# Kernel tuning notes

Measured on AMD Instinct MI355X. Metric: run time of the kernel, lower is better.

Reference implementation:

```python
import jax, jax.numpy as jnp
import numpy as np

FEATURE_DIM, HIDDEN_DIM, ATTN_DIM = 2048, 1024, 1024
B, L = 128, 196


def setup_inputs() -> dict:
    key = jax.random.key(0)
    ks = jax.random.split(key, 8)
    s_enc = 1.0 / np.sqrt(FEATURE_DIM)
    s_hid = 1.0 / np.sqrt(HIDDEN_DIM)
    s_full = 1.0 / np.sqrt(ATTN_DIM)
    return {
        "encoder_out": jax.random.normal(ks[0], (B, L, FEATURE_DIM), jnp.float32),
        "hidden": jax.random.normal(ks[1], (B, HIDDEN_DIM), jnp.float32),
        "W_enc": jax.random.uniform(ks[2], (FEATURE_DIM, ATTN_DIM), jnp.float32, -s_enc, s_enc),
        "b_enc": jax.random.uniform(ks[3], (ATTN_DIM,), jnp.float32, -s_enc, s_enc),
        "W_hid": jax.random.uniform(ks[4], (HIDDEN_DIM, ATTN_DIM), jnp.float32, -s_hid, s_hid),
        "b_hid": jax.random.uniform(ks[5], (ATTN_DIM,), jnp.float32, -s_hid, s_hid),
        "W_full": jax.random.uniform(ks[6], (ATTN_DIM,), jnp.float32, -s_full, s_full),
        "b_full": jax.random.uniform(ks[7], (1,), jnp.float32, -s_full, s_full),
    }


def reference(encoder_out, hidden, W_enc, b_enc, W_hid, b_hid, W_full, b_full):
    # attn1: (B, L, A)
    attn1 = jnp.einsum("blf,fa->bla", encoder_out, W_enc) + b_enc
    # attn2: (B, 1, A)
    attn2 = (hidden @ W_hid + b_hid)[:, None, :]
    attn = jax.nn.relu(attn1 + attn2)
    # scalar score per location: (B, L)
    scores = jnp.einsum("bla,a->bl", attn, W_full) + b_full[0]
    alpha = jax.nn.softmax(scores, axis=1)
    # weighted sum over L: (B, F)
    context = jnp.einsum("blf,bl->bf", encoder_out, alpha)
    return context, alpha
```

## Files before the change

kernel.cpp:

```cpp
#include <hip/hip_runtime.h>
#include <hip/hip_bf16.h>

typedef unsigned short u16;
typedef short s16x8 __attribute__((ext_vector_type(8)));
typedef unsigned int u32x4 __attribute__((ext_vector_type(4)));
typedef float f32x4 __attribute__((ext_vector_type(4)));

#define F_DIM 2048
#define A_DIM 1024
#define H_DIM 1024
#define BATCH 128
#define LLEN  196
#define MROWS (BATCH * LLEN)

__device__ __forceinline__ u16 f2b(float x) {
  union { float f; unsigned int u; } c; c.f = x;
  unsigned int r = (c.u + 0x7fffu + ((c.u >> 16) & 1u)) >> 16;
  return (u16)r;
}

__device__ __forceinline__ unsigned int f2b_pk(float a, float b) {
  unsigned int r;
  asm volatile("v_cvt_pk_bf16_f32 %0, %1, %2" : "=v"(r) : "v"(a), "v"(b));
  return r;
}

__device__ __forceinline__ void gload_lds16(const void* g, void* l) {
  __builtin_amdgcn_global_load_lds((const __attribute__((address_space(1))) void*)g,
                                   (__attribute__((address_space(3))) void*)l, 16, 0, 0);
}

__global__ void wenc_cvt_kernel(const float* __restrict__ W, u16* __restrict__ WT) {
  __shared__ float tile[32][33];
  int kb = blockIdx.x * 32, ab = blockIdx.y * 32;
  int t = threadIdx.x;
  int r = t >> 3, c = (t & 7) * 4;
  float4 v = *(const float4*)&W[(size_t)(kb + r) * A_DIM + ab + c];
  tile[r][c] = v.x; tile[r][c + 1] = v.y; tile[r][c + 2] = v.z; tile[r][c + 3] = v.w;
  __syncthreads();
  ushort4 o;
  o.x = f2b(tile[c + 0][r]);
  o.y = f2b(tile[c + 1][r]);
  o.z = f2b(tile[c + 2][r]);
  o.w = f2b(tile[c + 3][r]);
  *(ushort4*)&WT[(size_t)(ab + r) * F_DIM + kb + c] = o;
}

__global__ void attn2_kernel(const float* __restrict__ hidden, const float* __restrict__ W_hid,
                             const float* __restrict__ b_hid, const float* __restrict__ b_enc,
                             float* __restrict__ attn2p) {
  __shared__ float hl[8][128];
  int t = threadIdx.x;
  int a  = blockIdx.x * 256 + t;
  int b0 = blockIdx.y * 8;
  int k0 = blockIdx.z * 128;
  {
    int j = t >> 5, kk = (t & 31) * 4;
    float4 v = *(const float4*)&hidden[(size_t)(b0 + j) * H_DIM + k0 + kk];
    hl[j][kk + 0] = v.x; hl[j][kk + 1] = v.y; hl[j][kk + 2] = v.z; hl[j][kk + 3] = v.w;
  }
  __syncthreads();
  float acc[8] = {0.f, 0.f, 0.f, 0.f, 0.f, 0.f, 0.f, 0.f};
  #pragma unroll 4
  for (int k = 0; k < 128; ++k) {
    float w = W_hid[(size_t)(k0 + k) * A_DIM + a];
    #pragma unroll
    for (int j = 0; j < 8; ++j) acc[j] = fmaf(hl[j][k], w, acc[j]);
  }
  if (blockIdx.z == 0) {
    float bias = b_hid[a] + b_enc[a];
    #pragma unroll
    for (int j = 0; j < 8; ++j) acc[j] += bias;
  }
  #pragma unroll
  for (int j = 0; j < 8; ++j) atomicAdd(&attn2p[(size_t)(b0 + j) * A_DIM + a], acc[j]);
}

__global__ void gemm_score(const float* __restrict__ enc, const u16* __restrict__ WT,
                           const float* __restrict__ attn2p, const float* __restrict__ W_full,
                           float* __restrict__ scores) {
  __shared__ __align__(16) float Asf[128 * 32];
  __shared__ __align__(16) u16 Bs[128 * 32];
  __shared__ float wf_lds[128];
  __shared__ float at2_lds[2][128];

  int i = blockIdx.x;
  int g  = i >> 6;
  int r  = i & 63;
  int y  = r >> 3;
  int gi = r & 7;
  int mt = g * 8 + gi;
  if (mt >= MROWS / 128) return;

  int n0 = y * 128;
  int m0 = mt * 128;
  int t = threadIdx.x;

  int b0 = m0 / LLEN;
  int bnd = (b0 + 1) * LLEN;
  int b1 = min(b0 + 1, BATCH - 1);

  if (t < 128) {
    wf_lds[t] = W_full[n0 + t];
    at2_lds[0][t] = attn2p[(size_t)b0 * A_DIM + n0 + t];
    at2_lds[1][t] = attn2p[(size_t)b1 * A_DIM + n0 + t];
  }

  int lane = t & 63, wave = t >> 6;
  int wr = wave >> 1, wc = wave & 1;
  int c16 = lane & 15, quad = lane >> 4;

  f32x4 acc[4][4];
  #pragma unroll
  for (int ii = 0; ii < 4; ++ii)
    #pragma unroll
    for (int j = 0; j < 4; ++j) acc[ii][j] = (f32x4){0.f, 0.f, 0.f, 0.f};

  const float* agp = enc + (size_t)(m0 + wave * 32 + (lane >> 3)) * F_DIM
                         + ((lane & 7) ^ ((lane >> 3) & 7)) * 4;
  float* al = Asf + wave * 1024;
  const u16* bgp = WT + (size_t)(n0 + (t >> 2)) * F_DIM + ((t & 3) ^ ((t >> 3) & 3)) * 8;
  u16* bl = Bs + wave * 512;

  int akey = c16 & 7;
  int bkey = (c16 >> 1) & 3;

  for (int kt = 0; kt < F_DIM; kt += 32) {
    gload_lds16(agp + kt, al);
    gload_lds16(agp + (size_t)8 * F_DIM + kt, al + 256);
    gload_lds16(agp + (size_t)16 * F_DIM + kt, al + 512);
    gload_lds16(agp + (size_t)24 * F_DIM + kt, al + 768);
    gload_lds16(bgp + kt, bl);
    gload_lds16(bgp + (size_t)64 * F_DIM + kt, bl + 2048);
    __syncthreads();
    s16x8 af[4], bf[4];
    #pragma unroll
    for (int ii = 0; ii < 4; ++ii) {
      int arow = (wr * 64 + ii * 16 + c16) * 32;
      float4 lo = *(const float4*)&Asf[arow + ((2 * quad) ^ akey) * 4];
      float4 hi = *(const float4*)&Asf[arow + ((2 * quad + 1) ^ akey) * 4];
      u32x4 w;
      w.x = f2b_pk(lo.x, lo.y);
      w.y = f2b_pk(lo.z, lo.w);
      w.z = f2b_pk(hi.x, hi.y);
      w.w = f2b_pk(hi.z, hi.w);
      af[ii] = __builtin_bit_cast(s16x8, w);
      bf[ii] = *(const s16x8*)&Bs[(wc * 64 + ii * 16 + c16) * 32 + (quad ^ bkey) * 8];
    }
    #pragma unroll
    for (int mi = 0; mi < 4; ++mi)
      #pragma unroll
      for (int ni = 0; ni < 4; ++ni)
        acc[mi][ni] = __builtin_amdgcn_mfma_f32_16x16x32_bf16(af[mi], bf[ni], acc[mi][ni], 0, 0, 0);
    __syncthreads();
  }

  float wf[4], a2a[4], a2b[4];
  #pragma unroll
  for (int ni = 0; ni < 4; ++ni) {
    int col = wc * 64 + ni * 16 + c16;
    wf[ni] = wf_lds[col];
    a2a[ni] = at2_lds[0][col];
    a2b[ni] = at2_lds[1][col];
  }
  #pragma unroll
  for (int mi = 0; mi < 4; ++mi) {
    #pragma unroll
    for (int rr = 0; rr < 4; ++rr) {
      int row_g = m0 + wr * 64 + mi * 16 + quad * 4 + rr;
      bool hi = row_g >= bnd;
      float p = 0.f;
      #pragma unroll
      for (int ni = 0; ni < 4; ++ni) {
        float v = acc[mi][ni][rr] + (hi ? a2b[ni] : a2a[ni]);
        v = fmaxf(v, 0.f);
        p = fmaf(v, wf[ni], p);
      }
      p += __shfl_xor(p, 1);
      p += __shfl_xor(p, 2);
      p += __shfl_xor(p, 4);
      p += __shfl_xor(p, 8);
      if (c16 == 0) atomicAdd(&scores[row_g], p);
    }
  }
}

__global__ void softmax_kernel(const float* __restrict__ scores, float* __restrict__ alpha) {
  __shared__ float red[8];
  int b = blockIdx.x, t = threadIdx.x;
  float s = (t < LLEN) ? scores[b * LLEN + t] : -3.0e38f;
  float m = s;
  #pragma unroll
  for (int o = 1; o <= 32; o <<= 1) m = fmaxf(m, __shfl_xor(m, o));
  if ((t & 63) == 0) red[t >> 6] = m;
  __syncthreads();
  m = fmaxf(fmaxf(red[0], red[1]), fmaxf(red[2], red[3]));
  float e = (t < LLEN) ? expf(s - m) : 0.f;
  float sum = e;
  #pragma unroll
  for (int o = 1; o <= 32; o <<= 1) sum += __shfl_xor(sum, o);
  __syncthreads();
  if ((t & 63) == 0) red[4 + (t >> 6)] = sum;
  __syncthreads();
  sum = red[4] + red[5] + red[6] + red[7];
  if (t < LLEN) alpha[b * LLEN + t] = e / sum;
}

__global__ void context_kernel(const float* __restrict__ enc, const float* __restrict__ alpha,
                               float* __restrict__ out) {
  __shared__ float al[49];
  int b = blockIdx.y, t = threadIdx.x;
  int l0 = blockIdx.z * 49;
  int f4 = blockIdx.x * 256 + t;
  if (t < 49) al[t] = alpha[b * LLEN + l0 + t];
  __syncthreads();
  const float4* e4 = (const float4*)enc + ((size_t)b * LLEN + l0) * (F_DIM / 4) + f4;
  float4 acc = {0.f, 0.f, 0.f, 0.f};
  #pragma unroll 7
  for (int l = 0; l < 49; ++l) {
    float4 v = e4[(size_t)l * (F_DIM / 4)];
    float a = al[l];
    acc.x = fmaf(v.x, a, acc.x);
    acc.y = fmaf(v.y, a, acc.y);
    acc.z = fmaf(v.z, a, acc.z);
    acc.w = fmaf(v.w, a, acc.w);
  }
  float* o = out + (size_t)b * F_DIM + f4 * 4;
  atomicAdd(o + 0, acc.x);
  atomicAdd(o + 1, acc.y);
  atomicAdd(o + 2, acc.z);
  atomicAdd(o + 3, acc.w);
}

extern "C" void kernel_launch(void* const* d_in, const int* in_sizes, int n_in,
                              void* d_out, int out_size, void* d_ws, size_t ws_size,
                              hipStream_t stream) {
  const float* enc    = (const float*)d_in[0];
  const float* hidden = (const float*)d_in[1];
  const float* W_enc  = (const float*)d_in[2];
  const float* b_enc  = (const float*)d_in[3];
  const float* W_hid  = (const float*)d_in[4];
  const float* b_hid  = (const float*)d_in[5];
  const float* W_full = (const float*)d_in[6];
  float* out = (float*)d_out;
  float* alpha_out = out + (size_t)BATCH * F_DIM;

  const size_t wt_bytes = (size_t)A_DIM * F_DIM * sizeof(u16);
  const size_t a2_bytes = (size_t)BATCH * A_DIM * sizeof(float);
  const size_t sc_bytes = (size_t)MROWS * sizeof(float);
  char* ws = (char*)d_ws;
  u16*   WT     = (u16*)ws;
  float* attn2p = (float*)(ws + wt_bytes);
  float* scores = (float*)(ws + wt_bytes + a2_bytes);

  hipMemsetAsync(attn2p, 0, a2_bytes, stream);
  hipMemsetAsync(scores, 0, sc_bytes, stream);
  hipMemsetAsync(out, 0, (size_t)BATCH * F_DIM * sizeof(float), stream);

  wenc_cvt_kernel<<<dim3(F_DIM / 32, A_DIM / 32), 256, 0, stream>>>(W_enc, WT);
  attn2_kernel<<<dim3(A_DIM / 256, BATCH / 8, H_DIM / 128), 256, 0, stream>>>(hidden, W_hid, b_hid, b_enc, attn2p);
  gemm_score<<<dim3(1600), 256, 0, stream>>>(enc, WT, attn2p, W_full, scores);
  softmax_kernel<<<dim3(BATCH), 256, 0, stream>>>(scores, alpha_out);
  context_kernel<<<dim3(2, BATCH, 4), 256, 0, stream>>>(enc, alpha_out, out);
}
```

Measured before the change: 500.2 us.

## Merge prep kernels and memsets, convert A tile in registers, fuse softmax into context

The W_enc transpose, the attn2 GEMV (now full-K per block with no atomics), and zeroing of scores and out are merged into one prep kernel in place of separate launches and memsets. gemm_score now loads encoder rows into registers, converts them to bf16 and stores them to LDS, instead of using an async fp32 global-to-LDS copy with conversion at fragment load. The LDS XOR swizzles are removed. Softmax is fused into the context kernel, which recomputes it per block, cutting launch count and the alpha round trip. The risks are exposed global-load latency in the GEMM without async LDS loads, possible LDS bank conflicts without swizzling, and a less parallel attn2 (64 blocks doing full K).

```diff
diff --git a/kernel.cpp b/kernel.cpp
--- a/kernel.cpp
+++ b/kernel.cpp
@@ -13,6 +13,12 @@
 #define LLEN  196
 #define MROWS (BATCH * LLEN)
 
+#define PREP_WENC   2048
+#define PREP_ATTN2  (PREP_WENC + 64)
+#define PREP_ZSC    (PREP_ATTN2 + 25)
+#define PREP_ZOUT   (PREP_ZSC + 256)
+#define PREP_GRID   PREP_ZOUT
+
 __device__ __forceinline__ u16 f2b(float x) {
   union { float f; unsigned int u; } c; c.f = x;
   unsigned int r = (c.u + 0x7fffu + ((c.u >> 16) & 1u)) >> 16;
@@ -30,56 +36,60 @@
                                    (__attribute__((address_space(3))) void*)l, 16, 0, 0);
 }
 
-__global__ void wenc_cvt_kernel(const float* __restrict__ W, u16* __restrict__ WT) {
+__global__ void prep_kernel(const float* __restrict__ W, u16* __restrict__ WT,
+                            const float* __restrict__ hidden, const float* __restrict__ W_hid,
+                            const float* __restrict__ b_hid, const float* __restrict__ b_enc,
+                            float* __restrict__ attn2p, float* __restrict__ scores,
+                            float* __restrict__ out) {
   __shared__ float tile[32][33];
-  int kb = blockIdx.x * 32, ab = blockIdx.y * 32;
-  int t = threadIdx.x;
-  int r = t >> 3, c = (t & 7) * 4;
-  float4 v = *(const float4*)&W[(size_t)(kb + r) * A_DIM + ab + c];
-  tile[r][c] = v.x; tile[r][c + 1] = v.y; tile[r][c + 2] = v.z; tile[r][c + 3] = v.w;
-  __syncthreads();
-  ushort4 o;
-  o.x = f2b(tile[c + 0][r]);
-  o.y = f2b(tile[c + 1][r]);
-  o.z = f2b(tile[c + 2][r]);
-  o.w = f2b(tile[c + 3][r]);
-  *(ushort4*)&WT[(size_t)(ab + r) * F_DIM + kb + c] = o;
-}
-
-__global__ void attn2_kernel(const float* __restrict__ hidden, const float* __restrict__ W_hid,
-                             const float* __restrict__ b_hid, const float* __restrict__ b_enc,
-                             float* __restrict__ attn2p) {
-  __shared__ float hl[8][128];
-  int t = threadIdx.x;
-  int a  = blockIdx.x * 256 + t;
-  int b0 = blockIdx.y * 8;
-  int k0 = blockIdx.z * 128;
-  {
-    int j = t >> 5, kk = (t & 31) * 4;
-    float4 v = *(const float4*)&hidden[(size_t)(b0 + j) * H_DIM + k0 + kk];
-    hl[j][kk + 0] = v.x; hl[j][kk + 1] = v.y; hl[j][kk + 2] = v.z; hl[j][kk + 3] = v.w;
-  }
-  __syncthreads();
-  float acc[8] = {0.f, 0.f, 0.f, 0.f, 0.f, 0.f, 0.f, 0.f};
-  #pragma unroll 4
-  for (int k = 0; k < 128; ++k) {
-    float w = W_hid[(size_t)(k0 + k) * A_DIM + a];
-    #pragma unroll
-    for (int j = 0; j < 8; ++j) acc[j] = fmaf(hl[j][k], w, acc[j]);
-  }
-  if (blockIdx.z == 0) {
+  __shared__ float hl[8][1024];
+  int bid = blockIdx.x, t = threadIdx.x;
+
+  if (bid < PREP_WENC) {
+    int kb = (bid & 63) * 32, ab = (bid >> 6) * 32;
+    int r = t >> 3, c = (t & 7) * 4;
+    float4 v = *(const float4*)&W[(size_t)(kb + r) * A_DIM + ab + c];
+    tile[r][c] = v.x; tile[r][c + 1] = v.y; tile[r][c + 2] = v.z; tile[r][c + 3] = v.w;
+    __syncthreads();
+    ushort4 o;
+    o.x = f2b(tile[c + 0][r]);
+    o.y = f2b(tile[c + 1][r]);
+    o.z = f2b(tile[c + 2][r]);
+    o.w = f2b(tile[c + 3][r]);
+    *(ushort4*)&WT[(size_t)(ab + r) * F_DIM + kb + c] = o;
+  } else if (bid < PREP_ATTN2) {
+    int idx = bid - PREP_WENC;
+    int a  = (idx & 3) * 256 + t;
+    int b0 = (idx >> 2) * 8;
+    #pragma unroll
+    for (int j = 0; j < 8; ++j) {
+      float4 v = *(const float4*)&hidden[(size_t)(b0 + j) * H_DIM + t * 4];
+      *(float4*)&hl[j][t * 4] = v;
+    }
+    __syncthreads();
+    float acc[8] = {0.f, 0.f, 0.f, 0.f, 0.f, 0.f, 0.f, 0.f};
+    #pragma unroll 8
+    for (int k = 0; k < H_DIM; ++k) {
+      float w = W_hid[(size_t)k * A_DIM + a];
+      #pragma unroll
+      for (int j = 0; j < 8; ++j) acc[j] = fmaf(hl[j][k], w, acc[j]);
+    }
     float bias = b_hid[a] + b_enc[a];
     #pragma unroll
-    for (int j = 0; j < 8; ++j) acc[j] += bias;
-  }
-  #pragma unroll
-  for (int j = 0; j < 8; ++j) atomicAdd(&attn2p[(size_t)(b0 + j) * A_DIM + a], acc[j]);
+    for (int j = 0; j < 8; ++j) attn2p[(size_t)(b0 + j) * A_DIM + a] = acc[j] + bias;
+  } else if (bid < PREP_ZSC) {
+    int i4 = (bid - PREP_ATTN2) * 256 + t;
+    if (i4 < MROWS / 4) ((float4*)scores)[i4] = (float4){0.f, 0.f, 0.f, 0.f};
+  } else {
+    int i4 = (bid - PREP_ZSC) * 256 + t;
+    ((float4*)out)[i4] = (float4){0.f, 0.f, 0.f, 0.f};
+  }
 }
 
 __global__ void gemm_score(const float* __restrict__ enc, const u16* __restrict__ WT,
                            const float* __restrict__ attn2p, const float* __restrict__ W_full,
                            float* __restrict__ scores) {
-  __shared__ __align__(16) float Asf[128 * 32];
+  __shared__ __align__(16) u16 As[128 * 32];
   __shared__ __align__(16) u16 Bs[128 * 32];
   __shared__ float wf_lds[128];
   __shared__ float at2_lds[2][128];
@@ -116,36 +126,31 @@
     #pragma unroll
     for (int j = 0; j < 4; ++j) acc[ii][j] = (f32x4){0.f, 0.f, 0.f, 0.f};
 
-  const float* agp = enc + (size_t)(m0 + wave * 32 + (lane >> 3)) * F_DIM
-                         + ((lane & 7) ^ ((lane >> 3) & 7)) * 4;
-  float* al = Asf + wave * 1024;
-  const u16* bgp = WT + (size_t)(n0 + (t >> 2)) * F_DIM + ((t & 3) ^ ((t >> 3) & 3)) * 8;
+  const float* ap = enc + (size_t)(m0 + (t >> 2)) * F_DIM + (t & 3) * 8;
+  u16* aw = As + (t >> 2) * 32 + (t & 3) * 8;
+  const u16* bgp = WT + (size_t)(n0 + (t >> 2)) * F_DIM + (t & 3) * 8;
   u16* bl = Bs + wave * 512;
 
-  int akey = c16 & 7;
-  int bkey = (c16 >> 1) & 3;
-
   for (int kt = 0; kt < F_DIM; kt += 32) {
-    gload_lds16(agp + kt, al);
-    gload_lds16(agp + (size_t)8 * F_DIM + kt, al + 256);
-    gload_lds16(agp + (size_t)16 * F_DIM + kt, al + 512);
-    gload_lds16(agp + (size_t)24 * F_DIM + kt, al + 768);
     gload_lds16(bgp + kt, bl);
     gload_lds16(bgp + (size_t)64 * F_DIM + kt, bl + 2048);
+    float4 a0 = *(const float4*)(ap + kt);
+    float4 a1 = *(const float4*)(ap + kt + 4);
+    float4 a2 = *(const float4*)(ap + (size_t)64 * F_DIM + kt);
+    float4 a3 = *(const float4*)(ap + (size_t)64 * F_DIM + kt + 4);
+    u32x4 w0, w1;
+    w0.x = f2b_pk(a0.x, a0.y); w0.y = f2b_pk(a0.z, a0.w);
+    w0.z = f2b_pk(a1.x, a1.y); w0.w = f2b_pk(a1.z, a1.w);
+    w1.x = f2b_pk(a2.x, a2.y); w1.y = f2b_pk(a2.z, a2.w);
+    w1.z = f2b_pk(a3.x, a3.y); w1.w = f2b_pk(a3.z, a3.w);
+    *(u32x4*)aw = w0;
+    *(u32x4*)(aw + 64 * 32) = w1;
     __syncthreads();
     s16x8 af[4], bf[4];
     #pragma unroll
     for (int ii = 0; ii < 4; ++ii) {
-      int arow = (wr * 64 + ii * 16 + c16) * 32;
-      float4 lo = *(const float4*)&Asf[arow + ((2 * quad) ^ akey) * 4];
-      float4 hi = *(const float4*)&Asf[arow + ((2 * quad + 1) ^ akey) * 4];
-      u32x4 w;
-      w.x = f2b_pk(lo.x, lo.y);
-      w.y = f2b_pk(lo.z, lo.w);
-      w.z = f2b_pk(hi.x, hi.y);
-      w.w = f2b_pk(hi.z, hi.w);
-      af[ii] = __builtin_bit_cast(s16x8, w);
-      bf[ii] = *(const s16x8*)&Bs[(wc * 64 + ii * 16 + c16) * 32 + (quad ^ bkey) * 8];
+      af[ii] = *(const s16x8*)&As[(wr * 64 + ii * 16 + c16) * 32 + quad * 8];
+      bf[ii] = *(const s16x8*)&Bs[(wc * 64 + ii * 16 + c16) * 32 + quad * 8];
     }
     #pragma unroll
     for (int mi = 0; mi < 4; ++mi)
@@ -185,9 +190,13 @@
   }
 }
 
-__global__ void softmax_kernel(const float* __restrict__ scores, float* __restrict__ alpha) {
+__global__ void ctx_kernel(const float* __restrict__ enc, const float* __restrict__ scores,
+                           float* __restrict__ out) {
   __shared__ float red[8];
-  int b = blockIdx.x, t = threadIdx.x;
+  __shared__ float al[49];
+  int b = blockIdx.y, t = threadIdx.x;
+  int z = blockIdx.z;
+
   float s = (t < LLEN) ? scores[b * LLEN + t] : -3.0e38f;
   float m = s;
   #pragma unroll
@@ -203,27 +212,26 @@
   if ((t & 63) == 0) red[4 + (t >> 6)] = sum;
   __syncthreads();
   sum = red[4] + red[5] + red[6] + red[7];
-  if (t < LLEN) alpha[b * LLEN + t] = e / sum;
-}
-
-__global__ void context_kernel(const float* __restrict__ enc, const float* __restrict__ alpha,
-                               float* __restrict__ out) {
-  __shared__ float al[49];
-  int b = blockIdx.y, t = threadIdx.x;
-  int l0 = blockIdx.z * 49;
+  float a = e / sum;
+
+  if (blockIdx.x == 0 && z == 0 && t < LLEN)
+    out[(size_t)BATCH * F_DIM + b * LLEN + t] = a;
+
+  int l0 = z * 49;
+  if (t >= l0 && t < l0 + 49) al[t - l0] = a;
+  __syncthreads();
+
   int f4 = blockIdx.x * 256 + t;
-  if (t < 49) al[t] = alpha[b * LLEN + l0 + t];
-  __syncthreads();
   const float4* e4 = (const float4*)enc + ((size_t)b * LLEN + l0) * (F_DIM / 4) + f4;
   float4 acc = {0.f, 0.f, 0.f, 0.f};
   #pragma unroll 7
   for (int l = 0; l < 49; ++l) {
     float4 v = e4[(size_t)l * (F_DIM / 4)];
-    float a = al[l];
-    acc.x = fmaf(v.x, a, acc.x);
-    acc.y = fmaf(v.y, a, acc.y);
-    acc.z = fmaf(v.z, a, acc.z);
-    acc.w = fmaf(v.w, a, acc.w);
+    float aa = al[l];
+    acc.x = fmaf(v.x, aa, acc.x);
+    acc.y = fmaf(v.y, aa, acc.y);
+    acc.z = fmaf(v.z, aa, acc.z);
+    acc.w = fmaf(v.w, aa, acc.w);
   }
   float* o = out + (size_t)b * F_DIM + f4 * 4;
   atomicAdd(o + 0, acc.x);
@@ -243,23 +251,16 @@
   const float* b_hid  = (const float*)d_in[5];
   const float* W_full = (const float*)d_in[6];
   float* out = (float*)d_out;
-  float* alpha_out = out + (size_t)BATCH * F_DIM;
 
   const size_t wt_bytes = (size_t)A_DIM * F_DIM * sizeof(u16);
   const size_t a2_bytes = (size_t)BATCH * A_DIM * sizeof(float);
-  const size_t sc_bytes = (size_t)MROWS * sizeof(float);
   char* ws = (char*)d_ws;
   u16*   WT     = (u16*)ws;
   float* attn2p = (float*)(ws + wt_bytes);
   float* scores = (float*)(ws + wt_bytes + a2_bytes);
 
-  hipMemsetAsync(attn2p, 0, a2_bytes, stream);
-  hipMemsetAsync(scores, 0, sc_bytes, stream);
-  hipMemsetAsync(out, 0, (size_t)BATCH * F_DIM * sizeof(float), stream);
-
-  wenc_cvt_kernel<<<dim3(F_DIM / 32, A_DIM / 32), 256, 0, stream>>>(W_enc, WT);
-  attn2_kernel<<<dim3(A_DIM / 256, BATCH / 8, H_DIM / 128), 256, 0, stream>>>(hidden, W_hid, b_hid, b_enc, attn2p);
+  prep_kernel<<<dim3(PREP_GRID), 256, 0, stream>>>(W_enc, WT, hidden, W_hid, b_hid, b_enc,
+                                                   attn2p, scores, out);
   gemm_score<<<dim3(1600), 256, 0, stream>>>(enc, WT, attn2p, W_full, scores);
-  softmax_kernel<<<dim3(BATCH), 256, 0, stream>>>(scores, alpha_out);
-  context_kernel<<<dim3(2, BATCH, 4), 256, 0, stream>>>(enc, alpha_out, out);
-}
+  ctx_kernel<<<dim3(2, BATCH, 4), 256, 0, stream>>>(enc, scores, out);
+}
```

New measurement: 539.6 us. 1.08x slower.
